# Performance work log

Hardware: AMD Instinct MI355X
Metric: run time of the kernel (lower is better)

Reference implementation:

```python
import jax, jax.numpy as jnp
import numpy as np

N, E, M, F, L = 50000, 800000, 50000, 64, 20
HID = 32
NEG_SLOPE = 0.2


def gatv2(x, src, dst, Wl, Wr, att, b, heads, outc):
    # PyG GATv2Conv (eval mode, dropout off), self-loops already in src/dst.
    n = x.shape[0]
    xl = (x @ Wl).reshape(n, heads, outc)
    xr = (x @ Wr).reshape(n, heads, outc)
    e = jax.nn.leaky_relu(xl[src] + xr[dst], NEG_SLOPE)          # [E, H, C]
    score = jnp.einsum('ehc,hc->eh', e, att)                      # [E, H]
    smax = jax.ops.segment_max(score, dst, num_segments=n)
    ex = jnp.exp(score - smax[dst])
    denom = jax.ops.segment_sum(ex, dst, num_segments=n)
    alpha = ex / denom[dst]                                       # scatter-softmax
    out = jax.ops.segment_sum(alpha[:, :, None] * xl[src], dst, num_segments=n)
    return out.reshape(n, heads * outc) + b


def setup_inputs() -> dict:
    key = jax.random.key(0)
    ks = jax.random.split(key, 32)
    d = {}
    d['x'] = jax.random.normal(ks[0], (N, 60), jnp.float32)
    d['lane_x'] = jax.random.normal(ks[1], (M, 2), jnp.float32)
    d['centerline'] = jax.random.normal(ks[2], (F, L, 2), jnp.float32)
    d['edge_index'] = jax.random.randint(ks[3], (2, E), 0, N)
    d['focal_idx'] = jax.random.randint(ks[4], (F,), 0, N)
    s = 0.1
    d['emb_W'] = jax.random.normal(ks[5], (60, HID)) * s
    d['emb_b'] = jnp.zeros((HID,))
    d['c1_Wl'] = jax.random.normal(ks[6], (HID, 4 * HID)) * s
    d['c1_Wr'] = jax.random.normal(ks[7], (HID, 4 * HID)) * s
    d['c1_att'] = jax.random.normal(ks[8], (4, HID)) * s
    d['c1_b'] = jnp.zeros((4 * HID,))
    d['c2_Wl'] = jax.random.normal(ks[9], (4 * HID, 4 * HID)) * s
    d['c2_Wr'] = jax.random.normal(ks[10], (4 * HID, 4 * HID)) * s
    d['c2_att'] = jax.random.normal(ks[11], (4, HID)) * s
    d['c2_b'] = jnp.zeros((4 * HID,))
    d['map_W'] = jax.random.normal(ks[12], (2, HID)) * s
    d['map_b'] = jnp.zeros((HID,))
    d['gg_Wl'] = jax.random.normal(ks[13], (4 * HID, HID)) * s
    d['gg_Wr'] = jax.random.normal(ks[14], (4 * HID, HID)) * s
    d['gg_att'] = jax.random.normal(ks[15], (1, HID)) * s
    d['gg_b'] = jnp.zeros((HID,))
    d['cl_W'] = jax.random.normal(ks[16], (2, HID)) * s
    d['cl_b'] = jnp.zeros((HID,))
    d['fc1_W'] = jax.random.normal(ks[17], (3 * HID, HID)) * s
    d['fc1_b'] = jnp.zeros((HID,))
    d['fc2_W'] = jax.random.normal(ks[18], (HID, HID // 2)) * s
    d['fc2_b'] = jnp.zeros((HID // 2,))
    d['fco_W'] = jax.random.normal(ks[19], (HID // 2, 60)) * s
    d['fco_b'] = jnp.zeros((60,))
    return d


def reference(x, lane_x, centerline, edge_index, focal_idx,
              emb_W, emb_b, c1_Wl, c1_Wr, c1_att, c1_b,
              c2_Wl, c2_Wr, c2_att, c2_b, map_W, map_b,
              gg_Wl, gg_Wr, gg_att, gg_b, cl_W, cl_b,
              fc1_W, fc1_b, fc2_W, fc2_b, fco_W, fco_b):
    n = x.shape[0]
    loops = jnp.arange(n)
    src = jnp.concatenate([edge_index[0], loops])  # PyG adds self-loops
    dst = jnp.concatenate([edge_index[1], loops])
    # agent encoder + subgraph (two GATv2 layers, heads=4, concat)
    h = jax.nn.relu(x @ emb_W + emb_b)                                   # [N,32]
    h = jax.nn.relu(gatv2(h, src, dst, c1_Wl, c1_Wr, c1_att, c1_b, 4, HID))
    agent_feat = jax.nn.relu(gatv2(h, src, dst, c2_Wl, c2_Wr, c2_att, c2_b, 4, HID))  # [N,128]
    # map branch (executable path: no lane edges -> plain embedding + mean pool)
    map_x = jax.nn.relu(lane_x @ map_W + map_b)                          # [M,32]
    map_global = jnp.mean(map_x, axis=0, keepdims=True)                  # [1,32]
    # global graph (heads=1)
    gf = jax.nn.relu(gatv2(agent_feat, src, dst, gg_Wl, gg_Wr, gg_att, gg_b, 1, HID))  # [N,32]
    focal = gf[focal_idx]                                                # [F,32]
    map_g = jnp.broadcast_to(map_global, (focal.shape[0], HID))
    cl = jnp.mean(centerline, axis=1) @ cl_W + cl_b                      # [F,32]
    comb = jnp.concatenate([focal, map_g, cl], axis=1)                   # [F,96]
    h = jax.nn.relu(comb @ fc1_W + fc1_b)
    h = jax.nn.relu(h @ fc2_W + fc2_b)
    return h @ fco_W + fco_b                                             # [F,60]
```

## Files before the change

kernel.cpp:

```cpp
#include <hip/hip_runtime.h>
#include <hip/hip_bf16.h>
#include <hip/hip_fp16.h>

typedef _Float16 half_t;
typedef _Float16 h8 __attribute__((ext_vector_type(8)));
typedef _Float16 h4v __attribute__((ext_vector_type(4)));
typedef _Float16 h2v __attribute__((ext_vector_type(2)));
typedef float f4v __attribute__((ext_vector_type(4)));

union H8u { h8 v; h2v h2[4]; _Float16 e[8]; };
union H4u { h4v v; h2v h2[2]; _Float16 e[4]; };

static inline int cdiv(long a, long b) { return (int)((a + b - 1) / b); }

__device__ __forceinline__ void fma4(float4& a, float s, const float4& w) {
    a.x += s * w.x; a.y += s * w.y; a.z += s * w.z; a.w += s * w.w;
}

__device__ __forceinline__ h8 hmax8(h8 a, h8 b) {
#if __has_builtin(__builtin_elementwise_max)
    return __builtin_elementwise_max(a, b);
#else
    h8 r;
#pragma unroll
    for (int j = 0; j < 8; ++j) r[j] = (a[j] > b[j]) ? a[j] : b[j];
    return r;
#endif
}
__device__ __forceinline__ h4v hmax4(h4v a, h4v b) {
#if __has_builtin(__builtin_elementwise_max)
    return __builtin_elementwise_max(a, b);
#else
    h4v r;
#pragma unroll
    for (int j = 0; j < 4; ++j) r[j] = (a[j] > b[j]) ? a[j] : b[j];
    return r;
#endif
}

__device__ __forceinline__ float dot2acc(h2v a, h2v b, float c) {
#if __has_builtin(__builtin_amdgcn_fdot2)
    return __builtin_amdgcn_fdot2(a, b, c, false);
#else
    return c + (float)a.x * (float)b.x + (float)a.y * (float)b.y;
#endif
}


template <int K4, int C4, int R>
__global__ __launch_bounds__(256) void gemm_t_h(
        const float* __restrict__ X, const float* __restrict__ W,
        const float* __restrict__ bias, half_t* __restrict__ Y,
        int Nr, int relu) {
    int idx = blockIdx.x * blockDim.x + threadIdx.x;
    int total = (Nr / R) * C4;
    if (idx >= total) return;
    int c4 = idx % C4;
    int n0 = (idx / C4) * R;
    const float4* __restrict__ Wv = (const float4*)W;
    const float4* __restrict__ Xv = (const float4*)X;
    float4 acc[R];
    float4 binit = bias ? ((const float4*)bias)[c4] : make_float4(0.f, 0.f, 0.f, 0.f);
#pragma unroll
    for (int r = 0; r < R; ++r) acc[r] = binit;
#pragma unroll 4
    for (int k4 = 0; k4 < K4; ++k4) {
        float4 w0 = Wv[(size_t)(4 * k4 + 0) * C4 + c4];
        float4 w1 = Wv[(size_t)(4 * k4 + 1) * C4 + c4];
        float4 w2 = Wv[(size_t)(4 * k4 + 2) * C4 + c4];
        float4 w3 = Wv[(size_t)(4 * k4 + 3) * C4 + c4];
#pragma unroll
        for (int r = 0; r < R; ++r) {
            float4 xv = Xv[(size_t)(n0 + r) * K4 + k4];
            fma4(acc[r], xv.x, w0); fma4(acc[r], xv.y, w1);
            fma4(acc[r], xv.z, w2); fma4(acc[r], xv.w, w3);
        }
    }
#pragma unroll
    for (int r = 0; r < R; ++r) {
        float4 o = acc[r];
        if (relu) {
            o.x = fmaxf(o.x, 0.f); o.y = fmaxf(o.y, 0.f);
            o.z = fmaxf(o.z, 0.f); o.w = fmaxf(o.w, 0.f);
        }
        h4v oh; oh.x = (half_t)o.x; oh.y = (half_t)o.y; oh.z = (half_t)o.z; oh.w = (half_t)o.w;
        ((h4v*)Y)[(size_t)(n0 + r) * C4 + c4] = oh;
    }
}


__global__ void wtrans(const float* __restrict__ c1l, const float* __restrict__ c1r,
                       const float* __restrict__ c2l, const float* __restrict__ c2r,
                       const float* __restrict__ ggl, const float* __restrict__ ggr,
                       const float* __restrict__ at1, const float* __restrict__ at2,
                       const float* __restrict__ atg, half_t* __restrict__ dst) {
    int idx = blockIdx.x * blockDim.x + threadIdx.x;
    if (idx >= 49440) return;
    if (idx >= 49152) {
        int j = idx - 49152;
        float v = (j < 128) ? at1[j] : (j < 256) ? at2[j - 128] : atg[j - 256];
        dst[idx] = (half_t)v;
        return;
    }
    const float* src; int K, loc;
    if (idx < 8192) {
        K = 32;
        if (idx < 4096) { src = c1l; loc = idx; } else { src = c1r; loc = idx - 4096; }
        int k = loc % K, c = loc / K;
        dst[idx] = (half_t)src[k * 128 + c];
    } else if (idx < 40960) {
        K = 128;
        if (idx < 24576) { src = c2l; loc = idx - 8192; } else { src = c2r; loc = idx - 24576; }
        int k = loc % K, c = loc / K;
        dst[idx] = (half_t)src[k * 128 + c];
    } else {
        K = 128;
        if (idx < 45056) { src = ggl; loc = idx - 40960; } else { src = ggr; loc = idx - 45056; }
        int k = loc % K, c = loc / K;
        dst[idx] = (half_t)src[k * 32 + c];
    }
}


template <int K, int C1>
__global__ __launch_bounds__(256) void mfma_dual(
        const half_t* __restrict__ Xh,
        const half_t* __restrict__ W1t, const half_t* __restrict__ W2t,
        half_t* __restrict__ Y1, half_t* __restrict__ Y2, int Nr) {
    constexpr int KT = K / 32;
    constexpr int NBC = (2 * C1) / 64;
    int wave = threadIdx.x >> 6, lane = threadIdx.x & 63;
    int bCol = blockIdx.x % NBC;
    int bRow = blockIdx.x / NBC;
    int rowBase = bRow * 128 + wave * 32;
    int colBase = bCol * 64;
    int m = lane & 15, quad = lane >> 4;

    f4v acc[2][4] = {};

    const half_t* bptr[4];
#pragma unroll
    for (int nt = 0; nt < 4; ++nt) {
        int gc = colBase + nt * 16 + m;
        bptr[nt] = (gc < C1) ? (W1t + (size_t)gc * K) : (W2t + (size_t)(gc - C1) * K);
    }
    int r0 = rowBase + m, r1 = rowBase + 16 + m;
    int r0c = (r0 < Nr) ? r0 : (Nr - 1);
    int r1c = (r1 < Nr) ? r1 : (Nr - 1);
    const half_t* a0p = Xh + (size_t)r0c * K + quad * 8;
    const half_t* a1p = Xh + (size_t)r1c * K + quad * 8;

#pragma unroll
    for (int kk = 0; kk < KT; ++kk) {
        h8 a0 = *(const h8*)(a0p + kk * 32);
        h8 a1 = *(const h8*)(a1p + kk * 32);
#pragma unroll
        for (int nt = 0; nt < 4; ++nt) {
            h8 b = *(const h8*)(bptr[nt] + kk * 32 + quad * 8);
            acc[0][nt] = __builtin_amdgcn_mfma_f32_16x16x32_f16(a0, b, acc[0][nt], 0, 0, 0);
            acc[1][nt] = __builtin_amdgcn_mfma_f32_16x16x32_f16(a1, b, acc[1][nt], 0, 0, 0);
        }
    }

#pragma unroll
    for (int mt = 0; mt < 2; ++mt) {
#pragma unroll
        for (int nt = 0; nt < 4; ++nt) {
            int gc = colBase + nt * 16 + m;
            half_t* Y = (gc < C1) ? (Y1 + gc) : (Y2 + (gc - C1));
#pragma unroll
            for (int r = 0; r < 4; ++r) {
                int gr = rowBase + mt * 16 + quad * 4 + r;
                if (gr < Nr) Y[(size_t)gr * C1] = (half_t)acc[mt][nt][r];
            }
        }
    }
}


__global__ void count_dst(const int* __restrict__ ei, int* __restrict__ counts, int E) {
    int e = blockIdx.x * blockDim.x + threadIdx.x;
    if (e >= E) return;
    atomicAdd(&counts[ei[E + e]], 1);
}

#define SCAN_CH 2048

__global__ void reduce_chunks(const int* __restrict__ counts, int* __restrict__ partial, int N) {
    __shared__ int sh[256];
    int t = threadIdx.x, base = blockIdx.x * SCAN_CH + t * 8;
    int s = 0;
    for (int j = 0; j < 8; ++j) if (base + j < N) s += counts[base + j] + 1;
    sh[t] = s; __syncthreads();
    for (int off = 128; off >= 1; off >>= 1) {
        if (t < off) sh[t] += sh[t + off];
        __syncthreads();
    }
    if (t == 0) partial[blockIdx.x] = sh[0];
}

__global__ void scan_partials(int* __restrict__ partial, int nch) {
    if (threadIdx.x == 0 && blockIdx.x == 0) {
        int run = 0;
        for (int i = 0; i < nch; ++i) { int v = partial[i]; partial[i] = run; run += v; }
    }
}

__global__ void scan_chunks(int* __restrict__ counts, const int* __restrict__ partial,
                            int* __restrict__ offsets, int* __restrict__ cursor,
                            int* __restrict__ adj, int N) {
    __shared__ int sh[256];
    int t = threadIdx.x, b = blockIdx.x, base = b * SCAN_CH + t * 8;
    int v[8], s = 0;
    for (int j = 0; j < 8; ++j) {
        v[j] = (base + j < N) ? (counts[base + j] + 1) : 0;
        s += v[j];
    }
    sh[t] = s; __syncthreads();
    for (int off = 1; off < 256; off <<= 1) {
        int x = (t >= off) ? sh[t - off] : 0;
        __syncthreads();
        sh[t] += x;
        __syncthreads();
    }
    int run = partial[b] + (t == 0 ? 0 : sh[t - 1]);
    for (int j = 0; j < 8; ++j) {
        if (base + j < N) {
            offsets[base + j] = run;
            adj[run] = base + j;
            cursor[base + j] = run + 1;
            counts[base + j] = v[j];
        }
        run += v[j];
    }
}

__global__ __launch_bounds__(256) void fill_adj_sliced(
        const int* __restrict__ ei, int* __restrict__ cursor,
        int* __restrict__ adj, int E, int sliceSz) {
    int slice = blockIdx.x & 7;
    int lo = slice * sliceSz, hi = lo + sliceSz;
    int nb = gridDim.x >> 3;
    int bi = blockIdx.x >> 3;
    int stride = nb * 256;
    for (int e = bi * 256 + threadIdx.x; e < E; e += stride) {
        int d = ei[E + e];
        if (d >= lo && d < hi) {
            int pos = atomicAdd(&cursor[d], 1);
            adj[pos] = ei[e];
        }
    }
}


__global__ __launch_bounds__(256) void gat16_h4(
        const half_t* __restrict__ xl, const half_t* __restrict__ xr,
        const half_t* __restrict__ atth, const int* __restrict__ offsets,
        const int* __restrict__ counts, const int* __restrict__ adj,
        const float* __restrict__ bias, half_t* __restrict__ out, int N) {
    int wave = threadIdx.x >> 6, lane = threadIdx.x & 63;
    int g = lane >> 4, t = lane & 15;
    int d = blockIdx.x * 16 + wave * 4 + g;
    int dc = (d < N) ? d : (N - 1);
    int off = offsets[dc];
    int deg = (d < N) ? counts[dc] : 0;
    int dmax = deg;
    dmax = max(dmax, __shfl_xor(dmax, 16));
    dmax = max(dmax, __shfl_xor(dmax, 32));

    h8 xr8 = *(const h8*)(xr + (size_t)dc * 128 + t * 8);
    H8u at8; at8.v = *(const h8*)(atth + t * 8);

    float acc[8];
#pragma unroll
    for (int j = 0; j < 8; ++j) acc[j] = 0.f;
    float lsum = 0.f;
    h8 c02;
#pragma unroll
    for (int j = 0; j < 8; ++j) c02[j] = (half_t)0.2f;

    bool v0 = 0 < deg, v1 = 1 < deg, v2 = 2 < deg, v3 = 3 < deg;
    int s0 = adj[off];
    int s1 = adj[off + (v1 ? 1 : 0)];
    int s2 = adj[off + (v2 ? 2 : 0)];
    int s3 = adj[off + (v3 ? 3 : 0)];

    for (int i = 0; i < dmax; i += 4) {
        H8u a0, a1, a2, a3;
        a0.v = *(const h8*)(xl + (size_t)s0 * 128 + t * 8);
        a1.v = *(const h8*)(xl + (size_t)s1 * 128 + t * 8);
        a2.v = *(const h8*)(xl + (size_t)s2 * 128 + t * 8);
        a3.v = *(const h8*)(xl + (size_t)s3 * 128 + t * 8);
        int ni = i + 4;
        bool nv0 = ni < deg, nv1 = ni + 1 < deg, nv2 = ni + 2 < deg, nv3 = ni + 3 < deg;
        int n0 = adj[off + (nv0 ? ni : 0)];
        int n1 = adj[off + (nv1 ? ni + 1 : 0)];
        int n2 = adj[off + (nv2 ? ni + 2 : 0)];
        int n3 = adj[off + (nv3 ? ni + 3 : 0)];

        h8 e0 = a0.v + xr8, e1 = a1.v + xr8, e2 = a2.v + xr8, e3 = a3.v + xr8;
        H8u l0, l1, l2, l3;
        l0.v = hmax8(e0, e0 * c02);
        l1.v = hmax8(e1, e1 * c02);
        l2.v = hmax8(e2, e2 * c02);
        l3.v = hmax8(e3, e3 * c02);
        float p0 = 0.f, p1 = 0.f, p2 = 0.f, p3 = 0.f;
#pragma unroll
        for (int j = 0; j < 4; ++j) {
            p0 = dot2acc(l0.h2[j], at8.h2[j], p0);
            p1 = dot2acc(l1.h2[j], at8.h2[j], p1);
            p2 = dot2acc(l2.h2[j], at8.h2[j], p2);
            p3 = dot2acc(l3.h2[j], at8.h2[j], p3);
        }
        p0 += __shfl_xor(p0, 1); p1 += __shfl_xor(p1, 1);
        p2 += __shfl_xor(p2, 1); p3 += __shfl_xor(p3, 1);
        p0 += __shfl_xor(p0, 2); p1 += __shfl_xor(p1, 2);
        p2 += __shfl_xor(p2, 2); p3 += __shfl_xor(p3, 2);
        float w0 = v0 ? __expf(p0) : 0.f;
        float w1 = v1 ? __expf(p1) : 0.f;
        float w2 = v2 ? __expf(p2) : 0.f;
        float w3 = v3 ? __expf(p3) : 0.f;
        lsum += (w0 + w1) + (w2 + w3);
#pragma unroll
        for (int j = 0; j < 8; ++j)
            acc[j] += w0 * (float)a0.e[j] + w1 * (float)a1.e[j]
                    + w2 * (float)a2.e[j] + w3 * (float)a3.e[j];
        s0 = n0; s1 = n1; s2 = n2; s3 = n3;
        v0 = nv0; v1 = nv1; v2 = nv2; v3 = nv3;
    }

    if (d < N) {
        float inv = 1.f / lsum;
        H8u o;
#pragma unroll
        for (int j = 0; j < 8; ++j)
            o.e[j] = (half_t)fmaxf(acc[j] * inv + bias[t * 8 + j], 0.f);
        *(h8*)(out + (size_t)d * 128 + t * 8) = o.v;
    }
}

__global__ __launch_bounds__(256) void gat16_h1(
        const half_t* __restrict__ xl, const half_t* __restrict__ xr,
        const half_t* __restrict__ atth, const int* __restrict__ offsets,
        const int* __restrict__ counts, const int* __restrict__ adj,
        const float* __restrict__ bias, float* __restrict__ out, int N) {
    int wave = threadIdx.x >> 6, lane = threadIdx.x & 63;
    int g = lane >> 4, sub = (lane >> 3) & 1, t = lane & 7;
    int d = blockIdx.x * 16 + wave * 4 + g;
    int dc = (d < N) ? d : (N - 1);
    int off = offsets[dc];
    int deg = (d < N) ? counts[dc] : 0;
    int dmax = deg;
    dmax = max(dmax, __shfl_xor(dmax, 16));
    dmax = max(dmax, __shfl_xor(dmax, 32));

    h4v xr4 = *(const h4v*)(xr + (size_t)dc * 32 + t * 4);
    H4u at4; at4.v = *(const h4v*)(atth + t * 4);

    float acc[4] = {0.f, 0.f, 0.f, 0.f};
    float lsum = 0.f;
    h4v c02;
#pragma unroll
    for (int j = 0; j < 4; ++j) c02[j] = (half_t)0.2f;

    int i = sub;
    bool va = i < deg, vb = i + 2 < deg;
    int sa = adj[off + (va ? i : 0)];
    int sb = adj[off + (vb ? i + 2 : 0)];
    for (; i < dmax; i += 4) {
        H4u a, b;
        a.v = *(const h4v*)(xl + (size_t)sa * 32 + t * 4);
        b.v = *(const h4v*)(xl + (size_t)sb * 32 + t * 4);
        int ni = i + 4;
        bool nva = ni < deg, nvb = ni + 2 < deg;
        int na = adj[off + (nva ? ni : 0)];
        int nb = adj[off + (nvb ? ni + 2 : 0)];
        h4v ea = a.v + xr4, eb = b.v + xr4;
        H4u la, lb;
        la.v = hmax4(ea, ea * c02);
        lb.v = hmax4(eb, eb * c02);
        float pa = dot2acc(la.h2[0], at4.h2[0], 0.f);
        float pb = dot2acc(lb.h2[0], at4.h2[0], 0.f);
        pa = dot2acc(la.h2[1], at4.h2[1], pa);
        pb = dot2acc(lb.h2[1], at4.h2[1], pb);
        pa += __shfl_xor(pa, 1); pb += __shfl_xor(pb, 1);
        pa += __shfl_xor(pa, 2); pb += __shfl_xor(pb, 2);
        pa += __shfl_xor(pa, 4); pb += __shfl_xor(pb, 4);
        float wa = va ? __expf(pa) : 0.f;
        float wb = vb ? __expf(pb) : 0.f;
        lsum += wa + wb;
#pragma unroll
        for (int j = 0; j < 4; ++j)
            acc[j] += wa * (float)a.e[j] + wb * (float)b.e[j];
        sa = na; sb = nb; va = nva; vb = nvb;
    }

    lsum += __shfl_xor(lsum, 8);
#pragma unroll
    for (int j = 0; j < 4; ++j) acc[j] += __shfl_xor(acc[j], 8);

    if (d < N && sub == 0) {
        float inv = 1.f / lsum;
        float4 o;
        o.x = fmaxf(acc[0] * inv + bias[t * 4 + 0], 0.f);
        o.y = fmaxf(acc[1] * inv + bias[t * 4 + 1], 0.f);
        o.z = fmaxf(acc[2] * inv + bias[t * 4 + 2], 0.f);
        o.w = fmaxf(acc[3] * inv + bias[t * 4 + 3], 0.f);
        *(float4*)(out + (size_t)d * 32 + t * 4) = o;
    }
}


__global__ void map_sum_kernel(const float* __restrict__ lane_x, const float* __restrict__ map_W,
                               const float* __restrict__ map_b, float* __restrict__ sums, int M) {
    __shared__ float s[32];
    if (threadIdx.x < 32) s[threadIdx.x] = 0.f;
    __syncthreads();
    int t = blockIdx.x * blockDim.x + threadIdx.x;
    int nth = gridDim.x * blockDim.x;
    int c = t & 31;
    float w0 = map_W[c], w1 = map_W[32 + c], bb = map_b[c];
    float acc = 0.f;
    for (int m = t >> 5; m < M; m += nth >> 5) {
        float v = lane_x[(long)m * 2] * w0 + lane_x[(long)m * 2 + 1] * w1 + bb;
        acc += fmaxf(v, 0.f);
    }
    atomicAdd(&s[c], acc);
    __syncthreads();
    if (threadIdx.x < 32) atomicAdd(&sums[threadIdx.x], s[threadIdx.x]);
}


__global__ void head_kernel(const float* __restrict__ gf, const int* __restrict__ focal_idx,
                            const float* __restrict__ map_sums, int M,
                            const float* __restrict__ centerline, int L,
                            const float* __restrict__ cl_W, const float* __restrict__ cl_b,
                            const float* __restrict__ fc1_W, const float* __restrict__ fc1_b,
                            const float* __restrict__ fc2_W, const float* __restrict__ fc2_b,
                            const float* __restrict__ fco_W, const float* __restrict__ fco_b,
                            float* __restrict__ out) {
    int f = blockIdx.x;
    int lane = threadIdx.x;
    __shared__ float s_comb[96];
    __shared__ float s_h1[32];
    __shared__ float s_h2[16];
    __shared__ float s_cl[2];

    float c0 = 0.f, c1 = 0.f;
    if (lane < L) {
        c0 = centerline[((long)f * L + lane) * 2 + 0];
        c1 = centerline[((long)f * L + lane) * 2 + 1];
    }
    for (int off = 32; off >= 1; off >>= 1) {
        c0 += __shfl_down(c0, off);
        c1 += __shfl_down(c1, off);
    }
    if (lane == 0) { s_cl[0] = c0 / (float)L; s_cl[1] = c1 / (float)L; }
    __syncthreads();

    int fi = focal_idx[f];
    if (lane < 32) {
        s_comb[lane] = gf[(long)fi * 32 + lane];
        s_comb[32 + lane] = map_sums[lane] / (float)M;
        s_comb[64 + lane] = s_cl[0] * cl_W[lane] + s_cl[1] * cl_W[32 + lane] + cl_b[lane];
    }
    __syncthreads();

    if (lane < 32) {
        float acc = fc1_b[lane];
        for (int k = 0; k < 96; ++k) acc += s_comb[k] * fc1_W[k * 32 + lane];
        s_h1[lane] = fmaxf(acc, 0.f);
    }
    __syncthreads();

    if (lane < 16) {
        float acc = fc2_b[lane];
        for (int k = 0; k < 32; ++k) acc += s_h1[k] * fc2_W[k * 16 + lane];
        s_h2[lane] = fmaxf(acc, 0.f);
    }
    __syncthreads();

    if (lane < 60) {
        float acc = fco_b[lane];
        for (int k = 0; k < 16; ++k) acc += s_h2[k] * fco_W[k * 60 + lane];
        out[(long)f * 60 + lane] = acc;
    }
}


extern "C" void kernel_launch(void* const* d_in, const int* in_sizes, int n_in,
                              void* d_out, int out_size, void* d_ws, size_t ws_size,
                              hipStream_t stream) {
    const float* x          = (const float*)d_in[0];
    const float* lane_x     = (const float*)d_in[1];
    const float* centerline = (const float*)d_in[2];
    const int*   ei         = (const int*)d_in[3];
    const int*   focal_idx  = (const int*)d_in[4];
    const float* emb_W = (const float*)d_in[5];
    const float* emb_b = (const float*)d_in[6];
    const float* c1_Wl = (const float*)d_in[7];
    const float* c1_Wr = (const float*)d_in[8];
    const float* c1_att = (const float*)d_in[9];
    const float* c1_b  = (const float*)d_in[10];
    const float* c2_Wl = (const float*)d_in[11];
    const float* c2_Wr = (const float*)d_in[12];
    const float* c2_att = (const float*)d_in[13];
    const float* c2_b  = (const float*)d_in[14];
    const float* map_W = (const float*)d_in[15];
    const float* map_b = (const float*)d_in[16];
    const float* gg_Wl = (const float*)d_in[17];
    const float* gg_Wr = (const float*)d_in[18];
    const float* gg_att = (const float*)d_in[19];
    const float* gg_b  = (const float*)d_in[20];
    const float* cl_W  = (const float*)d_in[21];
    const float* cl_b  = (const float*)d_in[22];
    const float* fc1_W = (const float*)d_in[23];
    const float* fc1_b = (const float*)d_in[24];
    const float* fc2_W = (const float*)d_in[25];
    const float* fc2_b = (const float*)d_in[26];
    const float* fco_W = (const float*)d_in[27];
    const float* fco_b = (const float*)d_in[28];

    const int N = in_sizes[0] / 60;
    const int M = in_sizes[1] / 2;
    const int F = in_sizes[4];
    const int L = in_sizes[2] / (F * 2);
    const int E = in_sizes[3] / 2;
    const int Etot = E + N;

    half_t* Xl_h = (half_t*)d_ws;
    half_t* Xr_h = Xl_h + (size_t)N * 128;
    half_t* H0_h = Xr_h + (size_t)N * 128;
    half_t* H1_h = H0_h + (size_t)N * 32;
    half_t* AF_h = H1_h + (size_t)N * 128;
    float*  GF_f = (float*)(AF_h + (size_t)N * 128);
    half_t* Wt   = (half_t*)(GF_f + (size_t)N * 32);
    int* counts  = (int*)(Wt + 49440);
    int* offsets = counts + N;
    int* cursor  = offsets + N;
    int* adj     = cursor + N;
    float* MAPS  = (float*)(adj + Etot);
    int* partial = (int*)(MAPS + 32);

    half_t* c1Wlt = Wt + 0;
    half_t* c1Wrt = Wt + 4096;
    half_t* c2Wlt = Wt + 8192;
    half_t* c2Wrt = Wt + 24576;
    half_t* ggWlt = Wt + 40960;
    half_t* ggWrt = Wt + 45056;
    half_t* att1h = Wt + 49152;
    half_t* att2h = Wt + 49280;
    half_t* attgh = Wt + 49408;

    const int BS = 256;
    const int nch = cdiv(N, SCAN_CH);
    const int rowBlocks = cdiv(N, 128);
    const int sliceSz = cdiv(N, 8);

    hipMemsetAsync(counts, 0, (size_t)N * sizeof(int), stream);
    count_dst<<<cdiv(E, BS), BS, 0, stream>>>(ei, counts, E);
    reduce_chunks<<<nch, 256, 0, stream>>>(counts, partial, N);
    scan_partials<<<1, 64, 0, stream>>>(partial, nch);
    scan_chunks<<<nch, 256, 0, stream>>>(counts, partial, offsets, cursor, adj, N);
    fill_adj_sliced<<<8 * 104, 256, 0, stream>>>(ei, cursor, adj, E, sliceSz);

    wtrans<<<cdiv(49440, BS), BS, 0, stream>>>(c1_Wl, c1_Wr, c2_Wl, c2_Wr, gg_Wl, gg_Wr,
                                               c1_att, c2_att, gg_att, Wt);

    gemm_t_h<15, 8, 4><<<cdiv((long)(N / 4) * 8, BS), BS, 0, stream>>>(x, emb_W, emb_b, H0_h, N, 1);

    mfma_dual<32, 128><<<rowBlocks * 4, 256, 0, stream>>>(H0_h, c1Wlt, c1Wrt, Xl_h, Xr_h, N);
    gat16_h4<<<cdiv(N, 16), 256, 0, stream>>>(Xl_h, Xr_h, att1h, offsets, counts, adj, c1_b, H1_h, N);

    mfma_dual<128, 128><<<rowBlocks * 4, 256, 0, stream>>>(H1_h, c2Wlt, c2Wrt, Xl_h, Xr_h, N);
    gat16_h4<<<cdiv(N, 16), 256, 0, stream>>>(Xl_h, Xr_h, att2h, offsets, counts, adj, c2_b, AF_h, N);

    mfma_dual<128, 32><<<rowBlocks * 1, 256, 0, stream>>>(AF_h, ggWlt, ggWrt, Xl_h, Xr_h, N);
    gat16_h1<<<cdiv(N, 16), 256, 0, stream>>>(Xl_h, Xr_h, attgh, offsets, counts, adj, gg_b, GF_f, N);

    hipMemsetAsync(MAPS, 0, 32 * sizeof(float), stream);
    map_sum_kernel<<<64, BS, 0, stream>>>(lane_x, map_W, map_b, MAPS, M);

    head_kernel<<<F, 64, 0, stream>>>(GF_f, focal_idx, MAPS, M, centerline, L,
                                      cl_W, cl_b, fc1_W, fc1_b, fc2_W, fc2_b,
                                      fco_W, fco_b, (float*)d_out);
}
```

Baseline: 382.9 us.

## Sort each node's adjacency list and unroll heads=1 gather loop to four edges

Adds a per-node odd-even transposition sort of the CSR neighbor lists (up to 64 entries, one wave per node), so source gathers in every GAT layer visit rows in ascending order and get better cache locality. Separately, the heads=1 aggregation kernel now processes four edges per iteration instead of two, putting more independent gathers in flight. The sort costs an extra kernel with 64 shuffle rounds per node, and lists longer than 64 are only partly sorted. The wider unroll raises register use and wastes more lanes on low-degree nodes.

```diff
diff --git a/kernel.cpp b/kernel.cpp
--- a/kernel.cpp
+++ b/kernel.cpp
@@ -252,6 +252,27 @@
     }
 }
 
+__global__ __launch_bounds__(256) void sort_adj(
+        const int* __restrict__ offsets, const int* __restrict__ counts,
+        int* __restrict__ adj, int N) {
+    int wave = threadIdx.x >> 6, lane = threadIdx.x & 63;
+    int d = blockIdx.x * 4 + wave;
+    if (d >= N) return;
+    int off = offsets[d];
+    int deg = counts[d];
+    int m = (deg < 64) ? deg : 64;
+    int v = (lane < m) ? adj[off + lane] : 0x7fffffff;
+#pragma unroll 4
+    for (int r = 0; r < 64; ++r) {
+        int p;
+        if ((r & 1) == 0) p = lane ^ 1;
+        else p = (lane == 0 || lane == 63) ? lane : ((lane & 1) ? lane + 1 : lane - 1);
+        int pv = __shfl(v, p);
+        v = (lane < p) ? ((v < pv) ? v : pv) : ((lane > p) ? ((v > pv) ? v : pv) : v);
+    }
+    if (lane < m) adj[off + lane] = v;
+}
+
 
 __global__ __launch_bounds__(256) void gat16_h4(
         const half_t* __restrict__ xl, const half_t* __restrict__ xr,
@@ -364,35 +385,54 @@
     for (int j = 0; j < 4; ++j) c02[j] = (half_t)0.2f;
 
     int i = sub;
-    bool va = i < deg, vb = i + 2 < deg;
+    bool va = i < deg, vb = i + 2 < deg, vc = i + 4 < deg, vd = i + 6 < deg;
     int sa = adj[off + (va ? i : 0)];
     int sb = adj[off + (vb ? i + 2 : 0)];
-    for (; i < dmax; i += 4) {
-        H4u a, b;
+    int sc = adj[off + (vc ? i + 4 : 0)];
+    int sd = adj[off + (vd ? i + 6 : 0)];
+    for (; i < dmax; i += 8) {
+        H4u a, b, c, e;
         a.v = *(const h4v*)(xl + (size_t)sa * 32 + t * 4);
         b.v = *(const h4v*)(xl + (size_t)sb * 32 + t * 4);
-        int ni = i + 4;
-        bool nva = ni < deg, nvb = ni + 2 < deg;
+        c.v = *(const h4v*)(xl + (size_t)sc * 32 + t * 4);
+        e.v = *(const h4v*)(xl + (size_t)sd * 32 + t * 4);
+        int ni = i + 8;
+        bool nva = ni < deg, nvb = ni + 2 < deg, nvc = ni + 4 < deg, nvd = ni + 6 < deg;
         int na = adj[off + (nva ? ni : 0)];
         int nb = adj[off + (nvb ? ni + 2 : 0)];
-        h4v ea = a.v + xr4, eb = b.v + xr4;
-        H4u la, lb;
+        int nc = adj[off + (nvc ? ni + 4 : 0)];
+        int nd = adj[off + (nvd ? ni + 6 : 0)];
+        h4v ea = a.v + xr4, eb = b.v + xr4, ec = c.v + xr4, ed = e.v + xr4;
+        H4u la, lb, lc, ld;
         la.v = hmax4(ea, ea * c02);
         lb.v = hmax4(eb, eb * c02);
+        lc.v = hmax4(ec, ec * c02);
+        ld.v = hmax4(ed, ed * c02);
         float pa = dot2acc(la.h2[0], at4.h2[0], 0.f);
         float pb = dot2acc(lb.h2[0], at4.h2[0], 0.f);
+        float pc = dot2acc(lc.h2[0], at4.h2[0], 0.f);
+        float pd = dot2acc(ld.h2[0], at4.h2[0], 0.f);
         pa = dot2acc(la.h2[1], at4.h2[1], pa);
         pb = dot2acc(lb.h2[1], at4.h2[1], pb);
+        pc = dot2acc(lc.h2[1], at4.h2[1], pc);
+        pd = dot2acc(ld.h2[1], at4.h2[1], pd);
         pa += __shfl_xor(pa, 1); pb += __shfl_xor(pb, 1);
+        pc += __shfl_xor(pc, 1); pd += __shfl_xor(pd, 1);
         pa += __shfl_xor(pa, 2); pb += __shfl_xor(pb, 2);
+        pc += __shfl_xor(pc, 2); pd += __shfl_xor(pd, 2);
         pa += __shfl_xor(pa, 4); pb += __shfl_xor(pb, 4);
+        pc += __shfl_xor(pc, 4); pd += __shfl_xor(pd, 4);
         float wa = va ? __expf(pa) : 0.f;
         float wb = vb ? __expf(pb) : 0.f;
-        lsum += wa + wb;
+        float wc = vc ? __expf(pc) : 0.f;
+        float wd = vd ? __expf(pd) : 0.f;
+        lsum += (wa + wb) + (wc + wd);
 #pragma unroll
         for (int j = 0; j < 4; ++j)
-            acc[j] += wa * (float)a.e[j] + wb * (float)b.e[j];
-        sa = na; sb = nb; va = nva; vb = nvb;
+            acc[j] += wa * (float)a.e[j] + wb * (float)b.e[j]
+                    + wc * (float)c.e[j] + wd * (float)e.e[j];
+        sa = na; sb = nb; sc = nc; sd = nd;
+        va = nva; vb = nvb; vc = nvc; vd = nvd;
     }
 
     lsum += __shfl_xor(lsum, 8);
@@ -563,6 +603,7 @@
     scan_partials<<<1, 64, 0, stream>>>(partial, nch);
     scan_chunks<<<nch, 256, 0, stream>>>(counts, partial, offsets, cursor, adj, N);
     fill_adj_sliced<<<8 * 104, 256, 0, stream>>>(ei, cursor, adj, E, sliceSz);
+    sort_adj<<<cdiv(N, 4), 256, 0, stream>>>(offsets, counts, adj, N);
 
     wtrans<<<cdiv(49440, BS), BS, 0, stream>>>(c1_Wl, c1_Wr, c2_Wl, c2_Wr, gg_Wl, gg_Wr,
                                                c1_att, c2_att, gg_att, Wt);
```

New measurement: 418.7 us. 9.4% more time.
